# Performance work log

Hardware: AMD Instinct MI355X
Metric: run time of the kernel (lower is better)

## Reference

```python
import jax, jax.numpy as jnp
import numpy as np
from jax import lax

B, N, S, H = 8, 32, 512, 768   # batch, max spans, seq len, bert hidden
K, C, L = 3, 128, 64           # conv kernel height, cnn_hidden_size, num labels


def setup_inputs() -> dict:
    key = jax.random.key(0)
    ks = jax.random.split(key, 9)
    rng = np.random.default_rng(0)
    W = 16  # max span width
    starts = rng.integers(0, S - W, size=(B, N))
    widths = rng.integers(1, W + 1, size=(B, N))
    starts[0, 0], widths[0, 0] = 100, W        # force max span width = 16
    starts[0, 1], widths[0, 1] = S - W, 1      # force max prefix width = 496
    starts[0, 2], widths[0, 2] = 0, 1          # force min end = 1 -> max suffix = 511
    ends = starts + widths
    spans_dranges = jnp.asarray(np.stack([starts, ends], axis=-1), dtype=jnp.int32)
    sc = 0.02
    return {
        "tokens_emb": jax.random.normal(ks[0], (B, S, H), jnp.float32),
        "span_w": jax.random.normal(ks[1], (C, H, K), jnp.float32) * sc,
        "span_b": jax.random.normal(ks[2], (C,), jnp.float32) * sc,
        "prefix_w": jax.random.normal(ks[3], (C, H, K), jnp.float32) * sc,
        "prefix_b": jax.random.normal(ks[4], (C,), jnp.float32) * sc,
        "suffix_w": jax.random.normal(ks[5], (C, H, K), jnp.float32) * sc,
        "suffix_b": jax.random.normal(ks[6], (C,), jnp.float32) * sc,
        "fc_w": jax.random.normal(ks[7], (L, 3 * C), jnp.float32) * sc,
        "fc_b": jax.random.normal(ks[8], (L,), jnp.float32) * sc,
        "spans_dranges": spans_dranges,
        "word_seq_lengths": jnp.full((B,), S, dtype=jnp.int32),
        "max_span_width": W,
        "max_prefix_width": S - W,
        "max_suffix_width": S - 1,
    }


def _conv_pool(x, w, b):
    # x: [BN, T, H]; Conv2d(H->C, kernel (K,1)) over time + max_pool over all valid positions
    T = x.shape[1]
    if T < K:  # original pads with zeros up to kernel size
        x = jnp.pad(x, ((0, 0), (0, K - T), (0, 0)))
    y = lax.conv_general_dilated(x.transpose(0, 2, 1), w, (1,), 'VALID',
                                 dimension_numbers=('NCH', 'OIH', 'NCH'))  # [BN, C, T-K+1]
    return (y + b[None, :, None]).max(axis=2)  # pool_filter_size == full output length


def reference(tokens_emb, span_w, span_b, prefix_w, prefix_b, suffix_w, suffix_b,
              fc_w, fc_b, spans_dranges, word_seq_lengths,
              max_span_width, max_prefix_width, max_suffix_width):
    starts = spans_dranges[..., 0]  # [B,N]
    ends = spans_dranges[..., 1]

    def gather(idx, mask):
        # idx, mask: [B,N,W] -> zero-padded per-span token embeddings [B*N, W, H]
        g = jnp.take_along_axis(tokens_emb[:, None], jnp.clip(idx, 0, S - 1)[..., None], axis=2)
        return (g * mask[..., None]).reshape(B * N, -1, H)

    ar = jnp.arange(max_span_width)
    span_x = gather(starts[..., None] + ar, ar < (ends - starts)[..., None])
    arp = jnp.arange(max_prefix_width)
    prefix_x = gather(jnp.broadcast_to(arp, (B, N, max_prefix_width)), arp < starts[..., None])
    ars = jnp.arange(max_suffix_width)
    suffix_x = gather(ends[..., None] + ars,
                      ars < (word_seq_lengths[:, None, None] - ends[..., None]))

    feats = jnp.concatenate([
        _conv_pool(prefix_x, prefix_w, prefix_b),
        _conv_pool(span_x, span_w, span_b),
        _conv_pool(suffix_x, suffix_w, suffix_b),
    ], axis=-1)  # [B*N, 3C]
    probs = jax.nn.sigmoid(feats @ fc_w.T + fc_b)  # [B*N, L]
    pred_ids = (probs > 0.5).astype(jnp.int32).reshape(B, N, L)
    return probs, pred_ids
```

## Files before the change

### kernel.cpp

```cpp
#include <hip/hip_runtime.h>
#include <hip/hip_bf16.h>
#include <math.h>

#define NEG_INF (-1e30f)

typedef _Float16 half8 __attribute__((ext_vector_type(8)));
typedef _Float16 half4 __attribute__((ext_vector_type(4)));
typedef float f32x4 __attribute__((ext_vector_type(4)));

__device__ __forceinline__ void load_lds16(const void* g, void* l) {
  __builtin_amdgcn_global_load_lds((const __attribute__((address_space(1))) void*)g,
                                   (__attribute__((address_space(3))) void*)l, 16, 0, 0);
}

__global__ __launch_bounds__(256) void prep(
    const float* __restrict__ tokens, const float* __restrict__ span_w,
    const float* __restrict__ prefix_w, const float* __restrict__ suffix_w,
    const float* __restrict__ fc_w, _Float16* __restrict__ A2,
    _Float16* __restrict__ Bt, float* __restrict__ fcT) {
  int bid = blockIdx.x;
  int t = threadIdx.x;
  if (bid < 3072) {
    int g4 = (bid * 256 + t) * 4;
    int m = g4 / 768, h = g4 % 768;
    float4 x = *(const float4*)(tokens + g4);
    float xs[4] = {x.x, x.y, x.z, x.w};
    half4 hi, lo, hi6;
#pragma unroll
    for (int i = 0; i < 4; ++i) {
      _Float16 h_ = (_Float16)xs[i];
      hi[i] = h_;
      lo[i] = (_Float16)((xs[i] - (float)h_) * 64.0f);
      hi6[i] = (_Float16)((float)h_ * 0.015625f);
    }
    size_t base = (size_t)m * 2304 + h;
    *(half4*)(A2 + base) = hi;
    *(half4*)(A2 + base + 768) = lo;
    *(half4*)(A2 + base + 1536) = hi6;
  } else if (bid < 3216) {
    int g = (bid - 3072) * 256 + t;
    int ws = g / 12288;
    int r = g % 12288;
    int c = r / 96, h = (r % 96) * 8;
    const float* wsrc = (ws == 0) ? prefix_w : (ws == 1) ? span_w : suffix_w;
    const float* src = wsrc + (size_t)(c * 768 + h) * 3;
    float wv[24];
#pragma unroll
    for (int i = 0; i < 6; ++i) *(float4*)&wv[i * 4] = *(const float4*)(src + i * 4);
#pragma unroll
    for (int tap = 0; tap < 3; ++tap) {
      half8 hi, lo, hi6;
#pragma unroll
      for (int i = 0; i < 8; ++i) {
        float x = wv[i * 3 + tap];
        _Float16 h_ = (_Float16)x;
        hi[i] = h_;
        lo[i] = (_Float16)((x - (float)h_) * 64.0f);
        hi6[i] = (_Float16)((float)h_ * 0.015625f);
      }
      size_t jb = (size_t)(ws * 384 + tap * 128 + c) * 2304 + h;
      *(half8*)(Bt + jb) = hi;
      *(half8*)(Bt + jb + 768) = hi6;
      *(half8*)(Bt + jb + 1536) = lo;
    }
  } else {
    int g = (bid - 3216) * 256 + t;
    int i = g >> 6, c = g & 63;
    fcT[g] = fc_w[c * 384 + i];
  }
}

__global__ __launch_bounds__(256) void gemm_f16(const _Float16* __restrict__ A2,
                                                const _Float16* __restrict__ Bt,
                                                float* __restrict__ Ct) {
  __shared__ _Float16 As[2][64 * 64];
  __shared__ _Float16 Bs[2][128 * 64];
  const int bm = blockIdx.x * 64;
  const int bj = blockIdx.y * 128;
  const int tid = threadIdx.x;
  const int w = tid >> 6;
  const int lane = tid & 63;
  const int lr = lane >> 3;
  const int kcs = (lane & 7) ^ lr;
  const _Float16* gA = A2 + (size_t)(bm + w * 8 + lr) * 2304 + kcs * 8;
  const _Float16* gB = Bt + (size_t)(bj + w * 8 + lr) * 2304 + kcs * 8;
  const int mrow = lane & 15;
  const int qb = lane >> 4;
  const int sw = lane & 7;
  const int m0w = (w & 1) * 32;
  const int n0w = (w >> 1) * 64;
  const int co0 = (qb ^ sw) * 8;
  const int co1 = ((qb + 4) ^ sw) * 8;
  f32x4 acc[2][4];
#pragma unroll
  for (int i = 0; i < 2; ++i)
#pragma unroll
    for (int j = 0; j < 4; ++j) acc[i][j] = (f32x4){0.f, 0.f, 0.f, 0.f};

  load_lds16(gA, &As[0][w * 512]);
  load_lds16(gA + 32 * 2304, &As[0][2048 + w * 512]);
#pragma unroll
  for (int p = 0; p < 4; ++p)
    load_lds16(gB + (size_t)p * 32 * 2304, &Bs[0][p * 2048 + w * 512]);

  int cur = 0;
  for (int k0 = 0; k0 < 2304; k0 += 64) {
    __syncthreads();
    if (k0 + 64 < 2304) {
      int nxt = cur ^ 1;
      load_lds16(gA + k0 + 64, &As[nxt][w * 512]);
      load_lds16(gA + k0 + 64 + 32 * 2304, &As[nxt][2048 + w * 512]);
#pragma unroll
      for (int p = 0; p < 4; ++p)
        load_lds16(gB + k0 + 64 + (size_t)p * 32 * 2304,
                   &Bs[nxt][p * 2048 + w * 512]);
    }
#pragma unroll
    for (int ks = 0; ks < 2; ++ks) {
      const int co = ks ? co1 : co0;
      half8 a0 = *(const half8*)&As[cur][(m0w + mrow) * 64 + co];
      half8 a1 = *(const half8*)&As[cur][(m0w + 16 + mrow) * 64 + co];
#pragma unroll
      for (int nt = 0; nt < 4; ++nt) {
        half8 b = *(const half8*)&Bs[cur][(n0w + nt * 16 + mrow) * 64 + co];
        acc[0][nt] = __builtin_amdgcn_mfma_f32_16x16x32_f16(a0, b, acc[0][nt], 0, 0, 0);
        acc[1][nt] = __builtin_amdgcn_mfma_f32_16x16x32_f16(a1, b, acc[1][nt], 0, 0, 0);
      }
    }
    cur ^= 1;
  }
  const int mbase = bm + m0w + (lane >> 4) * 4;
#pragma unroll
  for (int mt = 0; mt < 2; ++mt)
#pragma unroll
    for (int nt = 0; nt < 4; ++nt) {
      int n_out = bj + n0w + nt * 16 + mrow;
      *(f32x4*)(Ct + (size_t)n_out * 4096 + mbase + mt * 16) = acc[mt][nt];
    }
}

__global__ __launch_bounds__(256) void scan_kernel(const float* __restrict__ Ct,
                                                   const int* __restrict__ wsl,
                                                   float* __restrict__ PM2,
                                                   float* __restrict__ SM2) {
  int pair = blockIdx.x * 4 + (threadIdx.x >> 6);
  int b = pair >> 7;
  int c = pair & 127;
  int lane = threadIdx.x & 63;
  int mb = b * 512;
  int t0 = lane * 8;
  const float* p0 = Ct + (size_t)(0 + c) * 4096 + mb;
  const float* p1 = Ct + (size_t)(128 + c) * 4096 + mb;
  const float* p2 = Ct + (size_t)(256 + c) * 4096 + mb;
  float v[8];
#pragma unroll
  for (int i = 0; i < 8; i++) {
    int t = t0 + i;
    v[i] = (t < 494) ? (p0[t] + p1[t + 1] + p2[t + 2]) : NEG_INF;
  }
#pragma unroll
  for (int i = 1; i < 8; i++) v[i] = fmaxf(v[i], v[i - 1]);
  float x = v[7];
#pragma unroll
  for (int d = 1; d < 64; d <<= 1) {
    float y = __shfl_up(x, d);
    if (lane >= d) x = fmaxf(x, y);
  }
  float excl = __shfl_up(x, 1);
  if (lane == 0) excl = NEG_INF;
  float* pm = PM2 + (size_t)pair * 512;
#pragma unroll
  for (int i = 0; i < 8; i++) {
    int t = t0 + i;
    if (t < 494) pm[t] = fmaxf(v[i], excl);
  }
  const float* s0 = Ct + (size_t)(768 + c) * 4096 + mb;
  const float* s1 = Ct + (size_t)(896 + c) * 4096 + mb;
  const float* s2 = Ct + (size_t)(1024 + c) * 4096 + mb;
  int qmax = wsl[b] - 3;
  if (qmax > 509) qmax = 509;
  float u[8];
#pragma unroll
  for (int i = 0; i < 8; i++) {
    int q = t0 + i;
    u[i] = (q <= qmax) ? (s0[q] + s1[q + 1] + s2[q + 2]) : NEG_INF;
  }
#pragma unroll
  for (int i = 6; i >= 0; i--) u[i] = fmaxf(u[i], u[i + 1]);
  float xr = u[0];
#pragma unroll
  for (int d = 1; d < 64; d <<= 1) {
    float y = __shfl_down(xr, d);
    if (lane < 64 - d) xr = fmaxf(xr, y);
  }
  float exclr = __shfl_down(xr, 1);
  if (lane == 63) exclr = NEG_INF;
  float* sm = SM2 + (size_t)pair * 512;
#pragma unroll
  for (int i = 0; i < 8; i++) sm[t0 + i] = fmaxf(u[i], exclr);
}

__global__ __launch_bounds__(128) void span_kernel(
    const float* __restrict__ Ct, const float* __restrict__ PM2,
    const float* __restrict__ SM2, const float* __restrict__ prefix_b,
    const float* __restrict__ span_b, const float* __restrict__ suffix_b,
    const float* __restrict__ fcT, const float* __restrict__ fc_b,
    const int* __restrict__ spans, const int* __restrict__ wsl,
    float* __restrict__ out) {
  __shared__ float sfeat[384];
  __shared__ float part[64];
  int sp = blockIdx.x;
  int b = sp >> 5;
  int c = threadIdx.x;
  int s = spans[sp * 2], e = spans[sp * 2 + 1];
  int Lb = wsl[b];
  int mb = b * 512;
  {
    const float* t0p = Ct + (size_t)c * 4096 + mb;
    const float* t1p = Ct + (size_t)(128 + c) * 4096 + mb;
    float m = NEG_INF;
    if (s >= 3) m = fmaxf(m, PM2[(size_t)(b * 128 + c) * 512 + s - 3]);
    if (s >= 2 && s <= 495) m = fmaxf(m, t0p[s - 2] + t1p[s - 1]);
    if (s >= 1 && s <= 494) m = fmaxf(m, t0p[s - 1]);
    if (s <= 493) m = fmaxf(m, 0.0f);
    sfeat[c] = m + prefix_b[c];
  }
  {
    const float* u0 = Ct + (size_t)(384 + c) * 4096 + mb;
    const float* u1 = Ct + (size_t)(512 + c) * 4096 + mb;
    const float* u2 = Ct + (size_t)(640 + c) * 4096 + mb;
    int w = e - s;
    float m = NEG_INF;
    for (int p = 0; p + 2 < w; ++p)
      m = fmaxf(m, u0[s + p] + u1[s + p + 1] + u2[s + p + 2]);
    if (w >= 2 && w <= 15) m = fmaxf(m, u0[s + w - 2] + u1[s + w - 1]);
    if (w <= 14) m = fmaxf(m, u0[s + w - 1]);
    if (w <= 13) m = fmaxf(m, 0.0f);
    sfeat[128 + c] = m + span_b[c];
  }
  {
    const float* x0 = Ct + (size_t)(768 + c) * 4096 + mb;
    const float* x1 = Ct + (size_t)(896 + c) * 4096 + mb;
    float m = NEG_INF;
    if (e <= Lb - 3) m = fmaxf(m, SM2[(size_t)(b * 128 + c) * 512 + e]);
    if (Lb - 2 - e >= 0 && Lb - 2 - e <= 508)
      m = fmaxf(m, x0[Lb - 2] + x1[Lb - 1]);
    if (Lb - 1 - e >= 0 && Lb - 1 - e <= 508) m = fmaxf(m, x0[Lb - 1]);
    if (Lb - e <= 508) m = fmaxf(m, 0.0f);
    sfeat[256 + c] = m + suffix_b[c];
  }
  __syncthreads();
  {
    int cc = threadIdx.x & 63;
    int half = threadIdx.x >> 6;
    float acc2 = 0.0f;
    const float* fp = fcT + (size_t)(half * 192) * 64 + cc;
    const float* sf = sfeat + half * 192;
#pragma unroll 8
    for (int i = 0; i < 192; ++i) acc2 = fmaf(sf[i], fp[(size_t)i * 64], acc2);
    if (half) part[cc] = acc2;
    __syncthreads();
    if (!half) {
      float a = acc2 + part[cc] + fc_b[cc];
      float pr = 1.0f / (1.0f + expf(-a));
      out[sp * 64 + cc] = pr;
      out[16384 + sp * 64 + cc] = (pr > 0.5f) ? 1.0f : 0.0f;
    }
  }
}

extern "C" void kernel_launch(void* const* d_in, const int* in_sizes, int n_in,
                              void* d_out, int out_size, void* d_ws,
                              size_t ws_size, hipStream_t stream) {
  const float* tokens = (const float*)d_in[0];
  const float* span_w = (const float*)d_in[1];
  const float* span_b = (const float*)d_in[2];
  const float* prefix_w = (const float*)d_in[3];
  const float* prefix_b = (const float*)d_in[4];
  const float* suffix_w = (const float*)d_in[5];
  const float* suffix_b = (const float*)d_in[6];
  const float* fc_w = (const float*)d_in[7];
  const float* fc_b = (const float*)d_in[8];
  const int* spans = (const int*)d_in[9];
  const int* wsl = (const int*)d_in[10];
  float* out = (float*)d_out;

  char* ws = (char*)d_ws;
  float* Ct = (float*)ws;
  _Float16* A2 = (_Float16*)(ws + 18874368);
  _Float16* Bt = (_Float16*)(ws + 37748736);
  float* PM2 = (float*)(ws + 43057152);
  float* SM2 = (float*)(ws + 45154304);
  float* fcT = (float*)(ws + 47251456);

  hipLaunchKernelGGL(prep, dim3(3312), dim3(256), 0, stream, tokens, span_w,
                     prefix_w, suffix_w, fc_w, A2, Bt, fcT);
  hipLaunchKernelGGL(gemm_f16, dim3(64, 9), dim3(256), 0, stream, A2, Bt, Ct);
  hipLaunchKernelGGL(scan_kernel, dim3(256), dim3(256), 0, stream, Ct, wsl,
                     PM2, SM2);
  hipLaunchKernelGGL(span_kernel, dim3(256), dim3(128), 0, stream, Ct, PM2,
                     SM2, prefix_b, span_b, suffix_b, fcT, fc_b, spans, wsl,
                     out);
}
```

Baseline: 153.3 us.

## Restructure GEMM to 128x64 tiles with register-staged two-deep prefetch

After: 482.0 us. +214.3%, slower.

```diff
diff --git a/kernel.cpp b/kernel.cpp
--- a/kernel.cpp
+++ b/kernel.cpp
@@ -7,11 +7,6 @@
 typedef _Float16 half8 __attribute__((ext_vector_type(8)));
 typedef _Float16 half4 __attribute__((ext_vector_type(4)));
 typedef float f32x4 __attribute__((ext_vector_type(4)));
-
-__device__ __forceinline__ void load_lds16(const void* g, void* l) {
-  __builtin_amdgcn_global_load_lds((const __attribute__((address_space(1))) void*)g,
-                                   (__attribute__((address_space(3))) void*)l, 16, 0, 0);
-}
 
 __global__ __launch_bounds__(256) void prep(
     const float* __restrict__ tokens, const float* __restrict__ span_w,
@@ -70,70 +65,81 @@
   }
 }
 
-__global__ __launch_bounds__(256) void gemm_f16(const _Float16* __restrict__ A2,
+__global__ __launch_bounds__(512) void gemm_f16(const _Float16* __restrict__ A2,
                                                 const _Float16* __restrict__ Bt,
                                                 float* __restrict__ Ct) {
-  __shared__ _Float16 As[2][64 * 64];
-  __shared__ _Float16 Bs[2][128 * 64];
-  const int bm = blockIdx.x * 64;
-  const int bj = blockIdx.y * 128;
+  __shared__ _Float16 As[2][128 * 64];
+  __shared__ _Float16 Bs[2][64 * 64];
+  const int bm = blockIdx.x * 128;
+  const int bj = blockIdx.y * 64;
   const int tid = threadIdx.x;
   const int w = tid >> 6;
   const int lane = tid & 63;
-  const int lr = lane >> 3;
-  const int kcs = (lane & 7) ^ lr;
-  const _Float16* gA = A2 + (size_t)(bm + w * 8 + lr) * 2304 + kcs * 8;
-  const _Float16* gB = Bt + (size_t)(bj + w * 8 + lr) * 2304 + kcs * 8;
+  const int sr = tid >> 3;
+  const int sc = tid & 7;
+  const _Float16* gA0 = A2 + (size_t)(bm + sr) * 2304 + sc * 8;
+  const _Float16* gA1 = A2 + (size_t)(bm + 64 + sr) * 2304 + sc * 8;
+  const _Float16* gB = Bt + (size_t)(bj + sr) * 2304 + sc * 8;
+  const int swz = (sc ^ (sr & 7)) * 8;
+  const int wa0 = sr * 64 + swz;
+  const int wa1 = (64 + sr) * 64 + swz;
+  const int wb = sr * 64 + swz;
   const int mrow = lane & 15;
   const int qb = lane >> 4;
-  const int sw = lane & 7;
-  const int m0w = (w & 1) * 32;
-  const int n0w = (w >> 1) * 64;
-  const int co0 = (qb ^ sw) * 8;
-  const int co1 = ((qb + 4) ^ sw) * 8;
-  f32x4 acc[2][4];
+  const int m0w = (w & 3) * 32;
+  const int n0w = (w >> 2) * 32;
+  const int co0 = (qb ^ (lane & 7)) * 8;
+  const int co1 = ((qb + 4) ^ (lane & 7)) * 8;
+  f32x4 acc[2][2];
 #pragma unroll
   for (int i = 0; i < 2; ++i)
 #pragma unroll
-    for (int j = 0; j < 4; ++j) acc[i][j] = (f32x4){0.f, 0.f, 0.f, 0.f};
-
-  load_lds16(gA, &As[0][w * 512]);
-  load_lds16(gA + 32 * 2304, &As[0][2048 + w * 512]);
-#pragma unroll
-  for (int p = 0; p < 4; ++p)
-    load_lds16(gB + (size_t)p * 32 * 2304, &Bs[0][p * 2048 + w * 512]);
-
-  int cur = 0;
-  for (int k0 = 0; k0 < 2304; k0 += 64) {
+    for (int j = 0; j < 2; ++j) acc[i][j] = (f32x4){0.f, 0.f, 0.f, 0.f};
+
+  half8 pA0[2], pA1[2], pB[2];
+  pA0[0] = *(const half8*)(gA0);
+  pA1[0] = *(const half8*)(gA1);
+  pB[0] = *(const half8*)(gB);
+  pA0[1] = *(const half8*)(gA0 + 64);
+  pA1[1] = *(const half8*)(gA1 + 64);
+  pB[1] = *(const half8*)(gB + 64);
+  *(half8*)&As[0][wa0] = pA0[0];
+  *(half8*)&As[0][wa1] = pA1[0];
+  *(half8*)&Bs[0][wb] = pB[0];
+
+  for (int i = 0; i < 36; ++i) {
+    const int cur = i & 1;
     __syncthreads();
-    if (k0 + 64 < 2304) {
-      int nxt = cur ^ 1;
-      load_lds16(gA + k0 + 64, &As[nxt][w * 512]);
-      load_lds16(gA + k0 + 64 + 32 * 2304, &As[nxt][2048 + w * 512]);
-#pragma unroll
-      for (int p = 0; p < 4; ++p)
-        load_lds16(gB + k0 + 64 + (size_t)p * 32 * 2304,
-                   &Bs[nxt][p * 2048 + w * 512]);
+    if (i + 2 < 36) {
+      const int k = (i + 2) * 64;
+      pA0[cur] = *(const half8*)(gA0 + k);
+      pA1[cur] = *(const half8*)(gA1 + k);
+      pB[cur] = *(const half8*)(gB + k);
     }
 #pragma unroll
     for (int ks = 0; ks < 2; ++ks) {
       const int co = ks ? co1 : co0;
       half8 a0 = *(const half8*)&As[cur][(m0w + mrow) * 64 + co];
       half8 a1 = *(const half8*)&As[cur][(m0w + 16 + mrow) * 64 + co];
-#pragma unroll
-      for (int nt = 0; nt < 4; ++nt) {
-        half8 b = *(const half8*)&Bs[cur][(n0w + nt * 16 + mrow) * 64 + co];
-        acc[0][nt] = __builtin_amdgcn_mfma_f32_16x16x32_f16(a0, b, acc[0][nt], 0, 0, 0);
-        acc[1][nt] = __builtin_amdgcn_mfma_f32_16x16x32_f16(a1, b, acc[1][nt], 0, 0, 0);
-      }
-    }
-    cur ^= 1;
-  }
-  const int mbase = bm + m0w + (lane >> 4) * 4;
+      half8 b0 = *(const half8*)&Bs[cur][(n0w + mrow) * 64 + co];
+      half8 b1 = *(const half8*)&Bs[cur][(n0w + 16 + mrow) * 64 + co];
+      acc[0][0] = __builtin_amdgcn_mfma_f32_16x16x32_f16(a0, b0, acc[0][0], 0, 0, 0);
+      acc[1][0] = __builtin_amdgcn_mfma_f32_16x16x32_f16(a1, b0, acc[1][0], 0, 0, 0);
+      acc[0][1] = __builtin_amdgcn_mfma_f32_16x16x32_f16(a0, b1, acc[0][1], 0, 0, 0);
+      acc[1][1] = __builtin_amdgcn_mfma_f32_16x16x32_f16(a1, b1, acc[1][1], 0, 0, 0);
+    }
+    if (i + 1 < 36) {
+      const int nb = cur ^ 1;
+      *(half8*)&As[nb][wa0] = pA0[nb];
+      *(half8*)&As[nb][wa1] = pA1[nb];
+      *(half8*)&Bs[nb][wb] = pB[nb];
+    }
+  }
+  const int mbase = bm + m0w + qb * 4;
 #pragma unroll
   for (int mt = 0; mt < 2; ++mt)
 #pragma unroll
-    for (int nt = 0; nt < 4; ++nt) {
+    for (int nt = 0; nt < 2; ++nt) {
       int n_out = bj + n0w + nt * 16 + mrow;
       *(f32x4*)(Ct + (size_t)n_out * 4096 + mbase + mt * 16) = acc[mt][nt];
     }
@@ -295,7 +301,7 @@
 
   hipLaunchKernelGGL(prep, dim3(3312), dim3(256), 0, stream, tokens, span_w,
                      prefix_w, suffix_w, fc_w, A2, Bt, fcT);
-  hipLaunchKernelGGL(gemm_f16, dim3(64, 9), dim3(256), 0, stream, A2, Bt, Ct);
+  hipLaunchKernelGGL(gemm_f16, dim3(32, 18), dim3(512), 0, stream, A2, Bt, Ct);
   hipLaunchKernelGGL(scan_kernel, dim3(256), dim3(256), 0, stream, Ct, wsl,
                      PM2, SM2);
   hipLaunchKernelGGL(span_kernel, dim3(256), dim3(128), 0, stream, Ct, PM2,
```

## Enlarge GEMM tile to 128x128 and pipeline via register-staged LDS loads

Applied to the files above, without the earlier changes.

Result: no change. 153.2 us (-0.1%).

```diff
diff --git a/kernel.cpp b/kernel.cpp
--- a/kernel.cpp
+++ b/kernel.cpp
@@ -7,11 +7,6 @@
 typedef _Float16 half8 __attribute__((ext_vector_type(8)));
 typedef _Float16 half4 __attribute__((ext_vector_type(4)));
 typedef float f32x4 __attribute__((ext_vector_type(4)));
-
-__device__ __forceinline__ void load_lds16(const void* g, void* l) {
-  __builtin_amdgcn_global_load_lds((const __attribute__((address_space(1))) void*)g,
-                                   (__attribute__((address_space(3))) void*)l, 16, 0, 0);
-}
 
 __global__ __launch_bounds__(256) void prep(
     const float* __restrict__ tokens, const float* __restrict__ span_w,
@@ -70,66 +65,99 @@
   }
 }
 
-__global__ __launch_bounds__(256) void gemm_f16(const _Float16* __restrict__ A2,
+__global__ __launch_bounds__(512) void gemm_f16(const _Float16* __restrict__ A2,
                                                 const _Float16* __restrict__ Bt,
                                                 float* __restrict__ Ct) {
-  __shared__ _Float16 As[2][64 * 64];
+  __shared__ _Float16 As[2][128 * 64];
   __shared__ _Float16 Bs[2][128 * 64];
-  const int bm = blockIdx.x * 64;
+  const int bm = blockIdx.x * 128;
   const int bj = blockIdx.y * 128;
   const int tid = threadIdx.x;
   const int w = tid >> 6;
   const int lane = tid & 63;
-  const int lr = lane >> 3;
-  const int kcs = (lane & 7) ^ lr;
-  const _Float16* gA = A2 + (size_t)(bm + w * 8 + lr) * 2304 + kcs * 8;
-  const _Float16* gB = Bt + (size_t)(bj + w * 8 + lr) * 2304 + kcs * 8;
+  const int r0 = tid >> 3, c0 = tid & 7;
+  const int r1 = (tid + 512) >> 3, c1 = tid & 7;
+  const _Float16* gA0 = A2 + (size_t)(bm + r0) * 2304 + c0 * 8;
+  const _Float16* gA1 = A2 + (size_t)(bm + r1) * 2304 + c1 * 8;
+  const _Float16* gB0 = Bt + (size_t)(bj + r0) * 2304 + c0 * 8;
+  const _Float16* gB1 = Bt + (size_t)(bj + r1) * 2304 + c1 * 8;
+  const int wa0 = r0 * 64 + ((c0 ^ (r0 & 7)) * 8);
+  const int wa1 = r1 * 64 + ((c1 ^ (r1 & 7)) * 8);
   const int mrow = lane & 15;
   const int qb = lane >> 4;
-  const int sw = lane & 7;
-  const int m0w = (w & 1) * 32;
-  const int n0w = (w >> 1) * 64;
-  const int co0 = (qb ^ sw) * 8;
-  const int co1 = ((qb + 4) ^ sw) * 8;
+  const int m0w = (w & 3) * 32;
+  const int n0w = (w >> 2) * 64;
+  const int co0 = (qb ^ (lane & 7)) * 8;
+  const int co1 = ((qb + 4) ^ (lane & 7)) * 8;
   f32x4 acc[2][4];
 #pragma unroll
   for (int i = 0; i < 2; ++i)
 #pragma unroll
     for (int j = 0; j < 4; ++j) acc[i][j] = (f32x4){0.f, 0.f, 0.f, 0.f};
 
-  load_lds16(gA, &As[0][w * 512]);
-  load_lds16(gA + 32 * 2304, &As[0][2048 + w * 512]);
-#pragma unroll
-  for (int p = 0; p < 4; ++p)
-    load_lds16(gB + (size_t)p * 32 * 2304, &Bs[0][p * 2048 + w * 512]);
-
-  int cur = 0;
-  for (int k0 = 0; k0 < 2304; k0 += 64) {
+  half8 sA0a, sA1a, sB0a, sB1a;
+  half8 sA0b, sA1b, sB0b, sB1b;
+  sA0a = *(const half8*)(gA0);
+  sA1a = *(const half8*)(gA1);
+  sB0a = *(const half8*)(gB0);
+  sB1a = *(const half8*)(gB1);
+  *(half8*)&As[0][wa0] = sA0a;
+  *(half8*)&As[0][wa1] = sA1a;
+  *(half8*)&Bs[0][wa0] = sB0a;
+  *(half8*)&Bs[0][wa1] = sB1a;
+  sA0b = *(const half8*)(gA0 + 64);
+  sA1b = *(const half8*)(gA1 + 64);
+  sB0b = *(const half8*)(gB0 + 64);
+  sB1b = *(const half8*)(gB1 + 64);
+
+#define COMPUTE_HALF(BUF, CO)                                                  \
+  {                                                                            \
+    half8 a0 = *(const half8*)&As[BUF][(m0w + mrow) * 64 + (CO)];              \
+    half8 a1 = *(const half8*)&As[BUF][(m0w + 16 + mrow) * 64 + (CO)];         \
+    _Pragma("unroll") for (int nt = 0; nt < 4; ++nt) {                         \
+      half8 b = *(const half8*)&Bs[BUF][(n0w + nt * 16 + mrow) * 64 + (CO)];   \
+      acc[0][nt] =                                                             \
+          __builtin_amdgcn_mfma_f32_16x16x32_f16(a0, b, acc[0][nt], 0, 0, 0);  \
+      acc[1][nt] =                                                             \
+          __builtin_amdgcn_mfma_f32_16x16x32_f16(a1, b, acc[1][nt], 0, 0, 0);  \
+    }                                                                          \
+  }
+
+  for (int i = 0; i < 36; i += 2) {
     __syncthreads();
-    if (k0 + 64 < 2304) {
-      int nxt = cur ^ 1;
-      load_lds16(gA + k0 + 64, &As[nxt][w * 512]);
-      load_lds16(gA + k0 + 64 + 32 * 2304, &As[nxt][2048 + w * 512]);
-#pragma unroll
-      for (int p = 0; p < 4; ++p)
-        load_lds16(gB + k0 + 64 + (size_t)p * 32 * 2304,
-                   &Bs[nxt][p * 2048 + w * 512]);
-    }
-#pragma unroll
-    for (int ks = 0; ks < 2; ++ks) {
-      const int co = ks ? co1 : co0;
-      half8 a0 = *(const half8*)&As[cur][(m0w + mrow) * 64 + co];
-      half8 a1 = *(const half8*)&As[cur][(m0w + 16 + mrow) * 64 + co];
-#pragma unroll
-      for (int nt = 0; nt < 4; ++nt) {
-        half8 b = *(const half8*)&Bs[cur][(n0w + nt * 16 + mrow) * 64 + co];
-        acc[0][nt] = __builtin_amdgcn_mfma_f32_16x16x32_f16(a0, b, acc[0][nt], 0, 0, 0);
-        acc[1][nt] = __builtin_amdgcn_mfma_f32_16x16x32_f16(a1, b, acc[1][nt], 0, 0, 0);
-      }
-    }
-    cur ^= 1;
-  }
-  const int mbase = bm + m0w + (lane >> 4) * 4;
+    if (i + 2 < 36) {
+      const int k = (i + 2) * 64;
+      sA0a = *(const half8*)(gA0 + k);
+      sA1a = *(const half8*)(gA1 + k);
+      sB0a = *(const half8*)(gB0 + k);
+      sB1a = *(const half8*)(gB1 + k);
+    }
+    COMPUTE_HALF(0, co0)
+    COMPUTE_HALF(0, co1)
+    *(half8*)&As[1][wa0] = sA0b;
+    *(half8*)&As[1][wa1] = sA1b;
+    *(half8*)&Bs[1][wa0] = sB0b;
+    *(half8*)&Bs[1][wa1] = sB1b;
+    __syncthreads();
+    if (i + 3 < 36) {
+      const int k = (i + 3) * 64;
+      sA0b = *(const half8*)(gA0 + k);
+      sA1b = *(const half8*)(gA1 + k);
+      sB0b = *(const half8*)(gB0 + k);
+      sB1b = *(const half8*)(gB1 + k);
+    }
+    COMPUTE_HALF(1, co0)
+    COMPUTE_HALF(1, co1)
+    if (i + 2 < 36) {
+      *(half8*)&As[0][wa0] = sA0a;
+      *(half8*)&As[0][wa1] = sA1a;
+      *(half8*)&Bs[0][wa0] = sB0a;
+      *(half8*)&Bs[0][wa1] = sB1a;
+    }
+  }
+#undef COMPUTE_HALF
+
+  const int mbase = bm + m0w + qb * 4;
 #pragma unroll
   for (int mt = 0; mt < 2; ++mt)
 #pragma unroll
@@ -295,7 +323,7 @@
 
   hipLaunchKernelGGL(prep, dim3(3312), dim3(256), 0, stream, tokens, span_w,
                      prefix_w, suffix_w, fc_w, A2, Bt, fcT);
-  hipLaunchKernelGGL(gemm_f16, dim3(64, 9), dim3(256), 0, stream, A2, Bt, Ct);
+  hipLaunchKernelGGL(gemm_f16, dim3(32, 9), dim3(512), 0, stream, A2, Bt, Ct);
   hipLaunchKernelGGL(scan_kernel, dim3(256), dim3(256), 0, stream, Ct, wsl,
                      PM2, SM2);
   hipLaunchKernelGGL(span_kernel, dim3(256), dim3(128), 0, stream, Ct, PM2,
```

## Drop redundant hi*2^-6 fp16 plane by reusing hi with separate low-order accumulator

Applied to the files above, without the earlier changes.

After: 149.3 us. 2.6% less time.

```diff
diff --git a/kernel.cpp b/kernel.cpp
--- a/kernel.cpp
+++ b/kernel.cpp
@@ -25,18 +25,16 @@
     int m = g4 / 768, h = g4 % 768;
     float4 x = *(const float4*)(tokens + g4);
     float xs[4] = {x.x, x.y, x.z, x.w};
-    half4 hi, lo, hi6;
+    half4 hi, lo;
 #pragma unroll
     for (int i = 0; i < 4; ++i) {
       _Float16 h_ = (_Float16)xs[i];
       hi[i] = h_;
       lo[i] = (_Float16)((xs[i] - (float)h_) * 64.0f);
-      hi6[i] = (_Float16)((float)h_ * 0.015625f);
-    }
-    size_t base = (size_t)m * 2304 + h;
+    }
+    size_t base = (size_t)m * 1536 + h;
     *(half4*)(A2 + base) = hi;
     *(half4*)(A2 + base + 768) = lo;
-    *(half4*)(A2 + base + 1536) = hi6;
   } else if (bid < 3216) {
     int g = (bid - 3072) * 256 + t;
     int ws = g / 12288;
@@ -49,19 +47,17 @@
     for (int i = 0; i < 6; ++i) *(float4*)&wv[i * 4] = *(const float4*)(src + i * 4);
 #pragma unroll
     for (int tap = 0; tap < 3; ++tap) {
-      half8 hi, lo, hi6;
+      half8 hi, lo;
 #pragma unroll
       for (int i = 0; i < 8; ++i) {
         float x = wv[i * 3 + tap];
         _Float16 h_ = (_Float16)x;
         hi[i] = h_;
         lo[i] = (_Float16)((x - (float)h_) * 64.0f);
-        hi6[i] = (_Float16)((float)h_ * 0.015625f);
       }
-      size_t jb = (size_t)(ws * 384 + tap * 128 + c) * 2304 + h;
+      size_t jb = (size_t)(ws * 384 + tap * 128 + c) * 1536 + h;
       *(half8*)(Bt + jb) = hi;
-      *(half8*)(Bt + jb + 768) = hi6;
-      *(half8*)(Bt + jb + 1536) = lo;
+      *(half8*)(Bt + jb + 768) = lo;
     }
   } else {
     int g = (bid - 3216) * 256 + t;
@@ -82,60 +78,68 @@
   const int lane = tid & 63;
   const int lr = lane >> 3;
   const int kcs = (lane & 7) ^ lr;
-  const _Float16* gA = A2 + (size_t)(bm + w * 8 + lr) * 2304 + kcs * 8;
-  const _Float16* gB = Bt + (size_t)(bj + w * 8 + lr) * 2304 + kcs * 8;
+  const int srcoff = (kcs >> 2) * 768 + (kcs & 3) * 8;
+  const _Float16* gA = A2 + (size_t)(bm + w * 8 + lr) * 1536 + srcoff;
+  const _Float16* gB = Bt + (size_t)(bj + w * 8 + lr) * 1536 + srcoff;
   const int mrow = lane & 15;
-  const int qb = lane >> 4;
-  const int sw = lane & 7;
+  const int q = lane >> 4;
   const int m0w = (w & 1) * 32;
   const int n0w = (w >> 1) * 64;
-  const int co0 = (qb ^ sw) * 8;
-  const int co1 = ((qb + 4) ^ sw) * 8;
-  f32x4 acc[2][4];
+  const int sw8 = mrow & 7;
+  const int coA0 = (q ^ sw8) * 8;
+  const int coA1 = ((q + 4) ^ sw8) * 8;
+  f32x4 aa[2][4], ab[2][4];
 #pragma unroll
   for (int i = 0; i < 2; ++i)
 #pragma unroll
-    for (int j = 0; j < 4; ++j) acc[i][j] = (f32x4){0.f, 0.f, 0.f, 0.f};
+    for (int j = 0; j < 4; ++j) {
+      aa[i][j] = (f32x4){0.f, 0.f, 0.f, 0.f};
+      ab[i][j] = (f32x4){0.f, 0.f, 0.f, 0.f};
+    }
 
   load_lds16(gA, &As[0][w * 512]);
-  load_lds16(gA + 32 * 2304, &As[0][2048 + w * 512]);
+  load_lds16(gA + 32 * 1536, &As[0][2048 + w * 512]);
 #pragma unroll
   for (int p = 0; p < 4; ++p)
-    load_lds16(gB + (size_t)p * 32 * 2304, &Bs[0][p * 2048 + w * 512]);
-
-  int cur = 0;
-  for (int k0 = 0; k0 < 2304; k0 += 64) {
+    load_lds16(gB + (size_t)p * 32 * 1536, &Bs[0][p * 2048 + w * 512]);
+
+  for (int i = 0; i < 24; ++i) {
+    const int cur = i & 1;
     __syncthreads();
-    if (k0 + 64 < 2304) {
-      int nxt = cur ^ 1;
-      load_lds16(gA + k0 + 64, &As[nxt][w * 512]);
-      load_lds16(gA + k0 + 64 + 32 * 2304, &As[nxt][2048 + w * 512]);
+    if (i + 1 < 24) {
+      const int kp = (i + 1) * 32;
+      const int nxt = cur ^ 1;
+      load_lds16(gA + kp, &As[nxt][w * 512]);
+      load_lds16(gA + kp + 32 * 1536, &As[nxt][2048 + w * 512]);
 #pragma unroll
       for (int p = 0; p < 4; ++p)
-        load_lds16(gB + k0 + 64 + (size_t)p * 32 * 2304,
+        load_lds16(gB + kp + (size_t)p * 32 * 1536,
                    &Bs[nxt][p * 2048 + w * 512]);
     }
-#pragma unroll
-    for (int ks = 0; ks < 2; ++ks) {
-      const int co = ks ? co1 : co0;
-      half8 a0 = *(const half8*)&As[cur][(m0w + mrow) * 64 + co];
-      half8 a1 = *(const half8*)&As[cur][(m0w + 16 + mrow) * 64 + co];
-#pragma unroll
-      for (int nt = 0; nt < 4; ++nt) {
-        half8 b = *(const half8*)&Bs[cur][(n0w + nt * 16 + mrow) * 64 + co];
-        acc[0][nt] = __builtin_amdgcn_mfma_f32_16x16x32_f16(a0, b, acc[0][nt], 0, 0, 0);
-        acc[1][nt] = __builtin_amdgcn_mfma_f32_16x16x32_f16(a1, b, acc[1][nt], 0, 0, 0);
-      }
-    }
-    cur ^= 1;
-  }
-  const int mbase = bm + m0w + (lane >> 4) * 4;
+    half8 a00 = *(const half8*)&As[cur][(m0w + mrow) * 64 + coA0];
+    half8 a01 = *(const half8*)&As[cur][(m0w + 16 + mrow) * 64 + coA0];
+    half8 a10 = *(const half8*)&As[cur][(m0w + mrow) * 64 + coA1];
+    half8 a11 = *(const half8*)&As[cur][(m0w + 16 + mrow) * 64 + coA1];
+#pragma unroll
+    for (int nt = 0; nt < 4; ++nt) {
+      half8 b0 = *(const half8*)&Bs[cur][(n0w + nt * 16 + mrow) * 64 + coA0];
+      half8 b1 = *(const half8*)&Bs[cur][(n0w + nt * 16 + mrow) * 64 + coA1];
+      aa[0][nt] = __builtin_amdgcn_mfma_f32_16x16x32_f16(a00, b0, aa[0][nt], 0, 0, 0);
+      aa[1][nt] = __builtin_amdgcn_mfma_f32_16x16x32_f16(a01, b0, aa[1][nt], 0, 0, 0);
+      ab[0][nt] = __builtin_amdgcn_mfma_f32_16x16x32_f16(a10, b0, ab[0][nt], 0, 0, 0);
+      ab[1][nt] = __builtin_amdgcn_mfma_f32_16x16x32_f16(a11, b0, ab[1][nt], 0, 0, 0);
+      ab[0][nt] = __builtin_amdgcn_mfma_f32_16x16x32_f16(a00, b1, ab[0][nt], 0, 0, 0);
+      ab[1][nt] = __builtin_amdgcn_mfma_f32_16x16x32_f16(a01, b1, ab[1][nt], 0, 0, 0);
+    }
+  }
+  const int mbase = bm + m0w + q * 4;
 #pragma unroll
   for (int mt = 0; mt < 2; ++mt)
 #pragma unroll
     for (int nt = 0; nt < 4; ++nt) {
       int n_out = bj + n0w + nt * 16 + mrow;
-      *(f32x4*)(Ct + (size_t)n_out * 4096 + mbase + mt * 16) = acc[mt][nt];
+      f32x4 v = aa[mt][nt] + 0.015625f * ab[mt][nt];
+      *(f32x4*)(Ct + (size_t)n_out * 4096 + mbase + mt * 16) = v;
     }
 }
 
@@ -288,10 +292,10 @@
   char* ws = (char*)d_ws;
   float* Ct = (float*)ws;
   _Float16* A2 = (_Float16*)(ws + 18874368);
-  _Float16* Bt = (_Float16*)(ws + 37748736);
-  float* PM2 = (float*)(ws + 43057152);
-  float* SM2 = (float*)(ws + 45154304);
-  float* fcT = (float*)(ws + 47251456);
+  _Float16* Bt = (_Float16*)(ws + 31457280);
+  float* PM2 = (float*)(ws + 34996224);
+  float* SM2 = (float*)(ws + 37093376);
+  float* fcT = (float*)(ws + 39190528);
 
   hipLaunchKernelGGL(prep, dim3(3312), dim3(256), 0, stream, tokens, span_w,
                      prefix_w, suffix_w, fc_w, A2, Bt, fcT);
```
